# Optimization experiments

Hardware: AMD Instinct MI355X
Metric: run time of the kernel (lower is better)

## Reference

```python
import jax, jax.numpy as jnp
import numpy as np

B, S, IN, E, H, FF, L = 8, 1024, 128, 512, 8, 2048, 4
HD = E // H
EPS = 1e-5


def make_pe(seq_len, d_model):
    position = np.arange(seq_len, dtype=np.float32)[:, None]
    div_term = np.exp(np.arange(0, d_model, 2, dtype=np.float32) * (-np.log(10000.0) / d_model))
    pe = np.zeros((seq_len, d_model), dtype=np.float32)
    pe[:, 0::2] = np.sin(position * div_term)
    pe[:, 1::2] = np.cos(position * div_term)
    return jnp.asarray(pe)


def setup_inputs() -> dict:
    key = jax.random.key(0)
    ks = jax.random.split(key, 16)
    s = 0.02
    return {
        "src": jax.random.normal(ks[0], (B, S, IN), jnp.float32),
        "distances": jax.random.uniform(ks[1], (B, S, S), jnp.float32),
        "proj_w": jax.random.normal(ks[2], (E, IN), jnp.float32) * s,
        "proj_b": jnp.zeros((E,), jnp.float32),
        "bn_g": jnp.ones((E,), jnp.float32),
        "bn_b": jnp.zeros((E,), jnp.float32),
        "in_proj_w": jax.random.normal(ks[3], (3 * E, E), jnp.float32) * s,
        "in_proj_b": jnp.zeros((3 * E,), jnp.float32),
        "dist_scale": jnp.array(1.0, jnp.float32),
        "lin1_w": jax.random.normal(ks[4], (FF, E), jnp.float32) * s,
        "lin1_b": jnp.zeros((FF,), jnp.float32),
        "lin2_w": jax.random.normal(ks[5], (E, FF), jnp.float32) * s,
        "lin2_b": jnp.zeros((E,), jnp.float32),
        "n1_g": jnp.ones((E,), jnp.float32),
        "n1_b": jnp.zeros((E,), jnp.float32),
        "n2_g": jnp.ones((E,), jnp.float32),
        "n2_b": jnp.zeros((E,), jnp.float32),
    }


def layernorm(x, g, b):
    m = jnp.mean(x, axis=-1, keepdims=True)
    v = jnp.var(x, axis=-1, keepdims=True)
    return (x - m) * jax.lax.rsqrt(v + EPS) * g + b


def reference(src, distances, proj_w, proj_b, bn_g, bn_b, in_proj_w, in_proj_b,
              dist_scale, lin1_w, lin1_b, lin2_w, lin2_b, n1_g, n1_b, n2_g, n2_b):
    # input projection
    x = jnp.einsum('bsi,ei->bse', src, proj_w) + proj_b  # [B,S,E]
    # BatchNorm1d over flattened (B*S) dim, training-mode batch stats
    xf = x.reshape(-1, E)
    mu = jnp.mean(xf, axis=0)
    var = jnp.var(xf, axis=0)
    x = ((xf - mu) * jax.lax.rsqrt(var + EPS) * bn_g + bn_b).reshape(B, S, E)
    # positional encoding
    x = x + make_pe(S, E)[None]
    # distance bias (same for every layer)
    dmax = jnp.max(distances, axis=-1, keepdims=True)
    dist_bias = jnp.exp(dist_scale * (1.0 - distances / dmax))  # [B,S,S]
    scale = 1.0 / jnp.sqrt(jnp.float32(HD))
    # num_layers iterations of the SAME (shared-parameter) layer
    for _ in range(L):
        qkv = jnp.einsum('bse,fe->bsf', x, in_proj_w) + in_proj_b  # [B,S,3E]
        q, k, v = jnp.split(qkv, 3, axis=-1)
        q = q.reshape(B, S, H, HD).transpose(0, 2, 1, 3)
        k = k.reshape(B, S, H, HD).transpose(0, 2, 1, 3)
        scores = jnp.einsum('bhqd,bhkd->bhqk', q, k) * scale  # [B,H,S,S]
        attn = jax.nn.softmax(scores, axis=-1)
        avg_w = jnp.mean(attn, axis=1)  # head-averaged weights [B,S,S]
        w = avg_w * dist_bias
        w = w / jnp.sum(w, axis=-1, keepdims=True)
        # NOTE: original bmm uses raw layer input as value (no V/out projection)
        attn_out = jnp.einsum('bqk,bke->bqe', w, x)
        x = layernorm(x + attn_out, n1_g, n1_b)
        ff = jnp.einsum('bsf,ef->bse', jax.nn.relu(jnp.einsum('bse,fe->bsf', x, lin1_w) + lin1_b), lin2_w) + lin2_b
        x = layernorm(x + ff, n2_g, n2_b)
    return x
```

## Files before the change

### kernel.cpp

```cpp
#include <hip/hip_runtime.h>
#include <hip/hip_bf16.h>
#include <math.h>

#define Bz 8
#define Sz 1024
#define INz 128
#define Ez 512
#define Hz 8
#define HDz 64
#define FFz 2048
#define Lz 4
#define Nz (Bz*Sz)
#define EPSf 1e-5f

typedef __attribute__((ext_vector_type(8))) short short8;
typedef __attribute__((ext_vector_type(4))) float floatx4;
#define MFMA16(a,b,c) __builtin_amdgcn_mfma_f32_16x16x32_bf16(a,b,c,0,0,0)

typedef __hip_bfloat16 bf16;

__device__ inline float b2f(bf16 v) { return __bfloat162float(v); }
__device__ inline bf16 f2b(float v) { return __float2bfloat16(v); }
__device__ inline float us2f(unsigned short u) { return __uint_as_float((unsigned)u << 16); }

__device__ inline void gload16(const bf16* g, bf16* lds_base)
{
  __builtin_amdgcn_global_load_lds(
      (const __attribute__((address_space(1))) void*)g,
      (__attribute__((address_space(3))) void*)lds_base,
      16, 0, 0);
}

#define FENCE() asm volatile("" ::: "memory")
#define PB() do { FENCE(); __builtin_amdgcn_s_barrier(); FENCE(); } while (0)
#define VMCNT0() asm volatile("s_waitcnt vmcnt(0)" ::: "memory")
#define VMCNT8() asm volatile("s_waitcnt vmcnt(8)" ::: "memory")

__global__ __launch_bounds__(256) void cast_f2b(const float* __restrict__ in,
    bf16* __restrict__ out, int n)
{
  int i = blockIdx.x * 256 + threadIdx.x;
  if (i < n) out[i] = f2b(in[i]);
}

__global__ __launch_bounds__(512, 1) void gemm256(
    const bf16* __restrict__ A, const bf16* __restrict__ Wm,
    const float* __restrict__ bias, bf16* __restrict__ Cb,
    int N, int K, int relu)
{
  int gx = gridDim.x, nwg = gx * gridDim.y;
  int flat = blockIdx.y * gx + blockIdx.x;
  if (!(nwg & 7)) {
    int cpx = nwg >> 3;
    flat = (flat & 7) * cpx + (flat >> 3);
  }
  int bm = (flat / gx) * 256, bn = (flat % gx) * 256;
  __shared__ __align__(16) bf16 As0[256][64], Bs0[256][64];
  __shared__ __align__(16) bf16 As1[256][64], Bs1[256][64];
  int t = threadIdx.x, wave = t >> 6, lane = t & 63;
  int wm = (wave >> 2) * 128, wn = (wave & 3) * 64;
  int fr = lane & 15, fo = lane >> 4;
  int w8 = wave * 8, lrow = lane >> 3;
  int sc8 = ((lane & 7) ^ (lrow & 7)) * 8;
  floatx4 acc[8][4];
  #pragma unroll
  for (int i = 0; i < 8; ++i)
    #pragma unroll
    for (int j = 0; j < 4; ++j) acc[i][j] = (floatx4){0.f, 0.f, 0.f, 0.f};

  #define STAGE8(DA, DB, kk) do {                                           \
    _Pragma("unroll")                                                        \
    for (int c_ = 0; c_ < 4; ++c_) {                                         \
      int row_ = c_ * 64 + w8 + lrow;                                        \
      gload16(A  + (size_t)(bm + row_) * K + (kk) + sc8, &DA[c_ * 64 + w8][0]);\
      gload16(Wm + (size_t)(bn + row_) * K + (kk) + sc8, &DB[c_ * 64 + w8][0]);\
    } } while (0)

  #define TILE(AA, BB, SA, SB, kk, DOSTAGE) do {                            \
    _Pragma("unroll")                                                        \
    for (int q_ = 0; q_ < 4; ++q_) {                                         \
      short8 a_[4][2], bf_[2][2];                                            \
      _Pragma("unroll")                                                      \
      for (int j_ = 0; j_ < 4; ++j_) {                                       \
        int row_ = wm + ((q_ >> 1) * 4 + j_) * 16 + fr;                      \
        a_[j_][0] = *(const short8*)&AA[row_][((fo) ^ (fr & 7)) * 8];        \
        a_[j_][1] = *(const short8*)&AA[row_][((4 + fo) ^ (fr & 7)) * 8];    \
      }                                                                      \
      _Pragma("unroll")                                                      \
      for (int g_ = 0; g_ < 2; ++g_) {                                       \
        int row_ = wn + ((q_ & 1) * 2 + g_) * 16 + fr;                       \
        bf_[g_][0] = *(const short8*)&BB[row_][((fo) ^ (fr & 7)) * 8];       \
        bf_[g_][1] = *(const short8*)&BB[row_][((4 + fo) ^ (fr & 7)) * 8];   \
      }                                                                      \
      if ((DOSTAGE) && q_ == 0) STAGE8(SA, SB, kk);                          \
      PB();                                                                  \
      __builtin_amdgcn_s_setprio(1);                                         \
      _Pragma("unroll")                                                      \
      for (int j_ = 0; j_ < 4; ++j_)                                         \
        _Pragma("unroll")                                                    \
        for (int g_ = 0; g_ < 2; ++g_) {                                     \
          int fi_ = (q_ >> 1) * 4 + j_, gi_ = (q_ & 1) * 2 + g_;             \
          acc[fi_][gi_] = MFMA16(a_[j_][0], bf_[g_][0], acc[fi_][gi_]);      \
          acc[fi_][gi_] = MFMA16(a_[j_][1], bf_[g_][1], acc[fi_][gi_]);      \
        }                                                                    \
      __builtin_amdgcn_s_setprio(0);                                         \
      if (q_ == 3) VMCNT0();                                                 \
      PB();                                                                  \
    } } while (0)

  int nt = K >> 6;
  STAGE8(As0, Bs0, 0);
  STAGE8(As1, Bs1, 64);
  VMCNT8();
  PB();
  TILE(As0, Bs0, As0, Bs0, 0, 0);
  for (int i = 1; i + 2 < nt; i += 2) {
    TILE(As1, Bs1, As0, Bs0, (i + 1) * 64, 1);
    TILE(As0, Bs0, As1, Bs1, (i + 2) * 64, 1);
  }
  TILE(As1, Bs1, As0, Bs0, 0, 0);
  #undef STAGE8
  #undef TILE

  #pragma unroll
  for (int f = 0; f < 8; ++f) {
    #pragma unroll
    for (int r = 0; r < 4; ++r) {
      int row = bm + wm + f * 16 + (lane >> 4) * 4 + r;
      #pragma unroll
      for (int g = 0; g < 4; ++g) {
        int col = bn + wn + g * 16 + fr;
        float v = acc[f][g][r] + (bias ? bias[col] : 0.f);
        if (relu) v = fmaxf(v, 0.f);
        Cb[(size_t)row * N + col] = f2b(v);
      }
    }
  }
}

__global__ __launch_bounds__(256) void gemm_bt(
    const bf16* __restrict__ A, const bf16* __restrict__ Wm,
    const float* __restrict__ bias, float* __restrict__ Cf,
    bf16* __restrict__ Cb, const float* __restrict__ rowscale,
    int M, int N, int K, int lda, int ldw,
    long sA, long sW, long sC, long sAk, long sWk, int nkc, int relu)
{
  int z = blockIdx.z;
  int bq = z / nkc, kc = z - bq * nkc;
  A  += (size_t)bq * sA + (size_t)kc * sAk;
  Wm += (size_t)bq * sW + (size_t)kc * sWk;
  if (rowscale) rowscale += (size_t)bq * M;
  size_t cbase = (size_t)bq * sC;
  const float* biasp = (kc == 0) ? bias : nullptr;
  int wrCf = (kc == 0), wrCb = (kc == nkc - 1);
  int bm = blockIdx.y * 128, bn = blockIdx.x * 128;
  __shared__ __align__(16) bf16 As0[128][64], Bs0[128][64];
  __shared__ __align__(16) bf16 As1[128][64], Bs1[128][64];
  int t = threadIdx.x, wave = t >> 6, lane = t & 63;
  int wm = (wave >> 1) * 64, wn = (wave & 1) * 64;
  int fr = lane & 15, fo = lane >> 4;
  int srow = lane >> 3;
  int scol = ((lane & 7) ^ srow) * 8;
  floatx4 acc[4][4];
  #pragma unroll
  for (int i = 0; i < 4; ++i)
    #pragma unroll
    for (int j = 0; j < 4; ++j) acc[i][j] = (floatx4){0.f, 0.f, 0.f, 0.f};

  #define STAGE(Ad, Bd, kk) do {                                            \
    _Pragma("unroll")                                                        \
    for (int i_ = 0; i_ < 4; ++i_) {                                         \
      int chunk_ = wave * 4 + i_;                                            \
      int row_ = chunk_ * 8 + srow;                                          \
      gload16(A  + (size_t)(bm + row_) * lda + (kk) + scol, &Ad[chunk_ * 8][0]);\
      gload16(Wm + (size_t)(bn + row_) * ldw + (kk) + scol, &Bd[chunk_ * 8][0]);\
    } } while (0)

  #define COMPUTE(Ad, Bd) do {                                               \
    _Pragma("unroll")                                                        \
    for (int ks_ = 0; ks_ < 2; ++ks_) {                                      \
      int sw_ = ((ks_ * 4 + fo) ^ (fr & 7)) * 8;                             \
      short8 af_[4], bf_[4];                                                 \
      _Pragma("unroll")                                                      \
      for (int rt_ = 0; rt_ < 4; ++rt_)                                      \
        af_[rt_] = *(const short8*)&Ad[wm + rt_ * 16 + fr][sw_];             \
      _Pragma("unroll")                                                      \
      for (int ct_ = 0; ct_ < 4; ++ct_)                                      \
        bf_[ct_] = *(const short8*)&Bd[wn + ct_ * 16 + fr][sw_];             \
      _Pragma("unroll")                                                      \
      for (int rt_ = 0; rt_ < 4; ++rt_)                                      \
        _Pragma("unroll")                                                    \
        for (int ct_ = 0; ct_ < 4; ++ct_)                                    \
          acc[rt_][ct_] = MFMA16(af_[rt_], bf_[ct_], acc[rt_][ct_]);         \
    } } while (0)

  STAGE(As0, Bs0, 0);
  __syncthreads();
  for (int k0 = 0; k0 < K; k0 += 128) {
    if (k0 + 64 < K) STAGE(As1, Bs1, k0 + 64);
    COMPUTE(As0, Bs0);
    __syncthreads();
    if (k0 + 64 < K) {
      if (k0 + 128 < K) STAGE(As0, Bs0, k0 + 128);
      COMPUTE(As1, Bs1);
      __syncthreads();
    }
  }
  #undef STAGE
  #undef COMPUTE

  #pragma unroll
  for (int rt = 0; rt < 4; ++rt) {
    #pragma unroll
    for (int r = 0; r < 4; ++r) {
      int row = bm + wm + rt * 16 + (lane >> 4) * 4 + r;
      float rs = rowscale ? (1.f / rowscale[row]) : 1.f;
      #pragma unroll
      for (int ct = 0; ct < 4; ++ct) {
        int col = bn + wn + ct * 16 + fr;
        float v = acc[rt][ct][r] + (biasp ? biasp[col] : 0.f);
        if (relu) v = fmaxf(v, 0.f);
        v *= rs;
        if (Cf && wrCf) Cf[cbase + (size_t)row * N + col] = v;
        if (Cb && wrCb) Cb[cbase + (size_t)row * N + col] = f2b(v);
      }
    }
  }
}

__global__ __launch_bounds__(256) void bn_stats(const float* __restrict__ x, float* __restrict__ st)
{
  int c = blockIdx.x;
  float s = 0.f, q = 0.f;
  for (int r = threadIdx.x; r < Nz; r += 256) {
    float v = x[(size_t)r * Ez + c];
    s += v; q += v * v;
  }
  for (int o = 32; o; o >>= 1) { s += __shfl_down(s, o); q += __shfl_down(q, o); }
  __shared__ float shs[4], shq[4];
  int w = threadIdx.x >> 6;
  if ((threadIdx.x & 63) == 0) { shs[w] = s; shq[w] = q; }
  __syncthreads();
  if (threadIdx.x == 0) {
    s = shs[0] + shs[1] + shs[2] + shs[3];
    q = shq[0] + shq[1] + shq[2] + shq[3];
    float mu = s / (float)Nz;
    float var = q / (float)Nz - mu * mu;
    st[c] = mu;
    st[Ez + c] = rsqrtf(var + EPSf);
  }
}

__global__ __launch_bounds__(256) void bn_apply_pe(const float* __restrict__ x0,
    const float* __restrict__ st, const float* __restrict__ g,
    const float* __restrict__ b, float* __restrict__ x, bf16* __restrict__ xb)
{
  int idx = blockIdx.x * 256 + threadIdx.x;
  int c = idx & (Ez - 1);
  int r = idx >> 9;
  int s = r & (Sz - 1);
  float dt = expf((float)(c & ~1) * (-9.210340371976184f / (float)Ez));
  float ang = (float)s * dt;
  float pe = (c & 1) ? cosf(ang) : sinf(ang);
  float mu = st[c], rs = st[Ez + c];
  float v = (x0[idx] - mu) * rs * g[c] + b[c] + pe;
  x[idx] = v;
  xb[idx] = f2b(v);
}

__global__ __launch_bounds__(256) void dist_bias_k(const float* __restrict__ dist,
    const float* __restrict__ dsc, bf16* __restrict__ db)
{
  size_t base = (size_t)blockIdx.x * Sz;
  float m = -1e30f;
  for (int j = threadIdx.x; j < Sz; j += 256) m = fmaxf(m, dist[base + j]);
  for (int o = 32; o; o >>= 1) m = fmaxf(m, __shfl_down(m, o));
  __shared__ float sh[4];
  if ((threadIdx.x & 63) == 0) sh[threadIdx.x >> 6] = m;
  __syncthreads();
  m = fmaxf(fmaxf(sh[0], sh[1]), fmaxf(sh[2], sh[3]));
  float sc = dsc[0];
  float inv = 1.f / m;
  for (int j = threadIdx.x; j < Sz; j += 256)
    db[base + j] = f2b(expf(sc * (1.f - dist[base + j] * inv)));
}

__global__ __launch_bounds__(256) void transpose_xb(const bf16* __restrict__ xb,
    bf16* __restrict__ xT)
{
  int b = blockIdx.z, e0 = blockIdx.y * 32, s0 = blockIdx.x * 32;
  __shared__ bf16 T[32][40];
  int t = threadIdx.x, row = t >> 3, c = t & 7;
  *(ushort4*)&T[row][c * 4] = *(const ushort4*)(xb + (size_t)(b * Sz + s0 + row) * Ez + e0 + c * 4);
  __syncthreads();
  ushort4 v;
  unsigned short* vp = (unsigned short*)&v;
  #pragma unroll
  for (int i = 0; i < 4; ++i) vp[i] = *(const unsigned short*)&T[c * 4 + i][row];
  *(ushort4*)(xT + ((size_t)b * Ez + e0 + row) * Sz + s0 + c * 4) = v;
}

__global__ __launch_bounds__(256) void attn_stats2(const bf16* __restrict__ qk,
    float* __restrict__ stats, float* __restrict__ den)
{
  int qt = blockIdx.x, h = blockIdx.y, b = blockIdx.z;
  int q0 = qt * 64;
  int t = threadIdx.x, wave = t >> 6, lane = t & 63;
  if (h == 0 && t < 64) den[(size_t)b * Sz + q0 + t] = 0.f;
  __shared__ bf16 Qs[64][72];
  __shared__ bf16 Ks[128][72];
  int fr = lane & 15, fo = (lane >> 4) * 8;
  #pragma unroll
  for (int i = 0; i < 2; ++i) {
    int idx = i * 256 + t, row = idx >> 3, c4 = idx & 7;
    *(float4*)&Qs[row][c4 * 8] =
      *(const float4*)(qk + (size_t)(b * Sz + q0 + row) * 1024 + h * 64 + c4 * 8);
  }
  __syncthreads();
  short8 aq0 = *(const short8*)&Qs[wave * 16 + fr][fo];
  short8 aq1 = *(const short8*)&Qs[wave * 16 + fr][32 + fo];
  float m_run[4] = {-1e30f, -1e30f, -1e30f, -1e30f};
  float z_run[4] = {0.f, 0.f, 0.f, 0.f};
  for (int k0 = 0; k0 < Sz; k0 += 128) {
    __syncthreads();
    #pragma unroll
    for (int i = 0; i < 4; ++i) {
      int idx = i * 256 + t, row = idx >> 3, c4 = idx & 7;
      *(float4*)&Ks[row][c4 * 8] =
        *(const float4*)(qk + (size_t)(b * Sz + k0 + row) * 1024 + 512 + h * 64 + c4 * 8);
    }
    __syncthreads();
    float sc[8][4];
    #pragma unroll
    for (int j = 0; j < 8; ++j) {
      floatx4 a4 = (floatx4){0.f, 0.f, 0.f, 0.f};
      short8 b0 = *(const short8*)&Ks[j * 16 + fr][fo];
      short8 b1 = *(const short8*)&Ks[j * 16 + fr][32 + fo];
      a4 = MFMA16(aq0, b0, a4);
      a4 = MFMA16(aq1, b1, a4);
      #pragma unroll
      for (int r = 0; r < 4; ++r) sc[j][r] = a4[r] * 0.125f;
    }
    #pragma unroll
    for (int r = 0; r < 4; ++r) {
      float vm = sc[0][r];
      #pragma unroll
      for (int j = 1; j < 8; ++j) vm = fmaxf(vm, sc[j][r]);
      #pragma unroll
      for (int o = 1; o < 16; o <<= 1) vm = fmaxf(vm, __shfl_xor(vm, o, 16));
      float mn = fmaxf(m_run[r], vm);
      float zb = 0.f;
      #pragma unroll
      for (int j = 0; j < 8; ++j) zb += __expf(sc[j][r] - mn);
      #pragma unroll
      for (int o = 1; o < 16; o <<= 1) zb += __shfl_xor(zb, o, 16);
      z_run[r] = z_run[r] * __expf(m_run[r] - mn) + zb;
      m_run[r] = mn;
    }
  }
  if (fr == 0) {
    int qb = q0 + wave * 16 + (lane >> 4) * 4;
    #pragma unroll
    for (int r = 0; r < 4; ++r) {
      size_t o = ((size_t)(b * Hz + h) * Sz + qb + r) * 2;
      stats[o] = m_run[r];
      stats[o + 1] = z_run[r];
    }
  }
}

__global__ __launch_bounds__(256) void scores_bias(const bf16* __restrict__ qk,
    const bf16* __restrict__ db, const float* __restrict__ stats,
    bf16* __restrict__ aw, float* __restrict__ den)
{
  int kt = blockIdx.x, qt = blockIdx.y, b = blockIdx.z;
  int q0 = qt * 128, k0 = kt * 128;
  __shared__ __align__(16) bf16 Qs0[128][64], Ks0[128][64];
  __shared__ __align__(16) bf16 Qs1[128][64], Ks1[128][64];
  __shared__ float mS[128][9];
  __shared__ float ziS[128][9];
  int t = threadIdx.x, wave = t >> 6, lane = t & 63;
  int fr = lane & 15, fo = lane >> 4;
  int wm = (wave >> 1) * 64, wn = (wave & 1) * 64;
  int srow = lane >> 3;
  int scol = ((lane & 7) ^ srow) * 8;
  int sw0 = ((fo) ^ (fr & 7)) * 8, sw1 = ((4 + fo) ^ (fr & 7)) * 8;

  #pragma unroll
  for (int i = 0; i < 4; ++i) {
    int lin = i * 256 + t, h = lin >> 7, q = lin & 127;
    const float* sp = stats + ((size_t)(b * Hz + h) * Sz + q0 + q) * 2;
    mS[q][h] = sp[0];
    ziS[q][h] = 1.f / sp[1];
  }

  floatx4 pac[4][4];
  #pragma unroll
  for (int i = 0; i < 4; ++i)
    #pragma unroll
    for (int j = 0; j < 4; ++j) pac[i][j] = (floatx4){0.f, 0.f, 0.f, 0.f};

  #define STAGEH(Qd, Kd, hh) do {                                            \
    _Pragma("unroll")                                                        \
    for (int i_ = 0; i_ < 4; ++i_) {                                         \
      int chunk_ = wave * 4 + i_, row_ = chunk_ * 8 + srow;                  \
      gload16(qk + (size_t)(b * Sz + q0 + row_) * 1024 + (hh) * 64 + scol,   \
              &Qd[chunk_ * 8][0]);                                           \
      gload16(qk + (size_t)(b * Sz + k0 + row_) * 1024 + 512 + (hh) * 64 + scol,\
              &Kd[chunk_ * 8][0]);                                           \
    } } while (0)

  #define HCOMP(Qd, Kd, hh) do {                                             \
    short8 bfv0[4], bfv1[4];                                                 \
    _Pragma("unroll")                                                        \
    for (int ct = 0; ct < 4; ++ct) {                                         \
      bfv0[ct] = *(const short8*)&Kd[wn + ct * 16 + fr][sw0];                \
      bfv1[ct] = *(const short8*)&Kd[wn + ct * 16 + fr][sw1];                \
    }                                                                        \
    _Pragma("unroll")                                                        \
    for (int rt = 0; rt < 4; ++rt) {                                         \
      short8 af0 = *(const short8*)&Qd[wm + rt * 16 + fr][sw0];              \
      short8 af1 = *(const short8*)&Qd[wm + rt * 16 + fr][sw1];              \
      floatx4 sc[4];                                                         \
      _Pragma("unroll")                                                      \
      for (int ct = 0; ct < 4; ++ct) {                                       \
        floatx4 z4 = (floatx4){0.f, 0.f, 0.f, 0.f};                          \
        z4 = MFMA16(af0, bfv0[ct], z4);                                      \
        sc[ct] = MFMA16(af1, bfv1[ct], z4);                                  \
      }                                                                      \
      _Pragma("unroll")                                                      \
      for (int r = 0; r < 4; ++r) {                                          \
        int qloc = wm + rt * 16 + (lane >> 4) * 4 + r;                       \
        float m = mS[qloc][hh], zi = ziS[qloc][hh];                          \
        _Pragma("unroll")                                                    \
        for (int ct = 0; ct < 4; ++ct)                                       \
          pac[rt][ct][r] += __expf(sc[ct][r] * 0.125f - m) * zi;             \
      }                                                                      \
    } } while (0)

  STAGEH(Qs0, Ks0, 0);
  __syncthreads();
  #pragma unroll 1
  for (int h = 0; h < 8; h += 2) {
    STAGEH(Qs1, Ks1, h + 1);
    HCOMP(Qs0, Ks0, h);
    __syncthreads();
    if (h + 2 < 8) STAGEH(Qs0, Ks0, h + 2);
    HCOMP(Qs1, Ks1, h + 1);
    __syncthreads();
  }
  #undef STAGEH
  #undef HCOMP

  #pragma unroll
  for (int rt = 0; rt < 4; ++rt) {
    #pragma unroll
    for (int r = 0; r < 4; ++r) {
      int qloc = wm + rt * 16 + (lane >> 4) * 4 + r;
      size_t rowoff = (size_t)(b * Sz + q0 + qloc) * Sz + k0;
      float rsum = 0.f;
      #pragma unroll
      for (int ct = 0; ct < 4; ++ct) {
        int kloc = wn + ct * 16 + fr;
        float p = pac[rt][ct][r] * 0.125f * b2f(db[rowoff + kloc]);
        aw[rowoff + kloc] = f2b(p);
        rsum += p;
      }
      #pragma unroll
      for (int o = 1; o < 16; o <<= 1) rsum += __shfl_xor(rsum, o, 16);
      if (fr == 0) atomicAdd(den + (size_t)b * Sz + q0 + qloc, rsum);
    }
  }
}

__global__ __launch_bounds__(256) void add_ln(const float* __restrict__ xin,
    const float* __restrict__ dly, const bf16* __restrict__ dly2,
    const float* __restrict__ g, const float* __restrict__ bb,
    float* __restrict__ xout, bf16* __restrict__ xbout)
{
  size_t base = (size_t)blockIdx.x * Ez;
  int t = threadIdx.x;
  float2 xi = *(const float2*)(xin + base + t * 2);
  float2 dl = *(const float2*)(dly + base + t * 2);
  float a0 = xi.x + dl.x;
  float a1 = xi.y + dl.y;
  if (dly2) {
    ushort2 u = *(const ushort2*)(dly2 + base + t * 2);
    a0 += us2f(u.x);
    a1 += us2f(u.y);
  }
  float s = a0 + a1, q = a0 * a0 + a1 * a1;
  for (int o = 32; o; o >>= 1) { s += __shfl_down(s, o); q += __shfl_down(q, o); }
  __shared__ float shs[4], shq[4];
  if ((t & 63) == 0) { shs[t >> 6] = s; shq[t >> 6] = q; }
  __syncthreads();
  s = shs[0] + shs[1] + shs[2] + shs[3];
  q = shq[0] + shq[1] + shq[2] + shq[3];
  float mu = s * (1.f / Ez);
  float var = q * (1.f / Ez) - mu * mu;
  float rs = rsqrtf(var + EPSf);
  float v0 = (a0 - mu) * rs * g[t * 2] + bb[t * 2];
  float v1 = (a1 - mu) * rs * g[t * 2 + 1] + bb[t * 2 + 1];
  float2 vo; vo.x = v0; vo.y = v1;
  *(float2*)(xout + base + t * 2) = vo;
  bf16 b0 = f2b(v0), b1 = f2b(v1);
  ushort2 pk;
  pk.x = *(unsigned short*)&b0;
  pk.y = *(unsigned short*)&b1;
  *(ushort2*)(xbout + base + t * 2) = pk;
}

extern "C" void kernel_launch(void* const* d_in, const int* in_sizes, int n_in,
                              void* d_out, int out_size, void* d_ws, size_t ws_size,
                              hipStream_t stream)
{
  const float* src        = (const float*)d_in[0];
  const float* distances  = (const float*)d_in[1];
  const float* proj_w     = (const float*)d_in[2];
  const float* proj_b     = (const float*)d_in[3];
  const float* bn_g       = (const float*)d_in[4];
  const float* bn_b       = (const float*)d_in[5];
  const float* in_proj_w  = (const float*)d_in[6];
  const float* in_proj_b  = (const float*)d_in[7];
  const float* dist_scale = (const float*)d_in[8];
  const float* lin1_w     = (const float*)d_in[9];
  const float* lin1_b     = (const float*)d_in[10];
  const float* lin2_w     = (const float*)d_in[11];
  const float* lin2_b     = (const float*)d_in[12];
  const float* n1_g       = (const float*)d_in[13];
  const float* n1_b       = (const float*)d_in[14];
  const float* n2_g       = (const float*)d_in[15];
  const float* n2_b       = (const float*)d_in[16];

  float* x = (float*)d_out;

  float* stats = (float*)d_ws;
  float* den   = stats + 131072;
  float* bnst  = den + 8192;
  float* aout  = bnst + 1024;
  float* x0    = aout;
  bf16* db_b = (bf16*)(aout + (size_t)Nz * Ez);
  bf16* Rqk  = db_b + (size_t)Bz * Sz * Sz;
  bf16* qk   = Rqk;
  bf16* aw   = Rqk + (size_t)Nz * 1024;
  bf16* ff1  = Rqk;
  bf16* xb   = Rqk + (size_t)Nz * FFz;
  bf16* xT   = xb + (size_t)Nz * Ez;
  bf16* srcb = xT + (size_t)Bz * Ez * Sz;
  bf16* wpr  = srcb + (size_t)Nz * INz;
  bf16* wqk  = wpr + Ez * INz;
  bf16* wl1  = wqk + 1024 * Ez;
  bf16* wl2  = wl1 + FFz * Ez;
  bf16* pvs2 = qk;
  bf16* ffs2 = xT;

  cast_f2b<<<(Nz * INz) / 256, 256, 0, stream>>>(src, srcb, Nz * INz);
  cast_f2b<<<(Ez * INz + 255) / 256, 256, 0, stream>>>(proj_w, wpr, Ez * INz);
  cast_f2b<<<(1024 * Ez) / 256, 256, 0, stream>>>(in_proj_w, wqk, 1024 * Ez);
  cast_f2b<<<(FFz * Ez) / 256, 256, 0, stream>>>(lin1_w, wl1, FFz * Ez);
  cast_f2b<<<(Ez * FFz) / 256, 256, 0, stream>>>(lin2_w, wl2, Ez * FFz);

  gemm_bt<<<dim3(Ez / 128, Nz / 128, 1), 256, 0, stream>>>(
      srcb, wpr, proj_b, x0, nullptr, nullptr,
      Nz, Ez, INz, INz, INz, 0, 0, 0, 0, 0, 1, 0);
  bn_stats<<<Ez, 256, 0, stream>>>(x0, bnst);
  bn_apply_pe<<<(Nz * Ez) / 256, 256, 0, stream>>>(x0, bnst, bn_g, bn_b, x, xb);
  dist_bias_k<<<Bz * Sz, 256, 0, stream>>>(distances, dist_scale, db_b);

  for (int l = 0; l < Lz; ++l) {
    transpose_xb<<<dim3(Sz / 32, Ez / 32, Bz), 256, 0, stream>>>(xb, xT);
    gemm_bt<<<dim3(1024 / 128, Nz / 128, 1), 256, 0, stream>>>(
        xb, wqk, in_proj_b, nullptr, qk, nullptr,
        Nz, 1024, Ez, Ez, Ez, 0, 0, 0, 0, 0, 1, 0);
    attn_stats2<<<dim3(Sz / 64, Hz, Bz), 256, 0, stream>>>(qk, stats, den);
    scores_bias<<<dim3(Sz / 128, Sz / 128, Bz), 256, 0, stream>>>(qk, db_b, stats, aw, den);
    gemm_bt<<<dim3(Ez / 128, Sz / 128, Bz * 2), 256, 0, stream>>>(
        aw, xT, nullptr, aout, pvs2, den,
        Sz, Ez, 512, Sz, Sz,
        (long)Sz * Sz, (long)Ez * Sz, (long)Sz * Ez, 512, 512, 2, 0);
    add_ln<<<Nz, 256, 0, stream>>>(x, aout, pvs2, n1_g, n1_b, x, xb);
    gemm256<<<dim3(FFz / 256, Nz / 256), 512, 0, stream>>>(
        xb, wl1, lin1_b, ff1, FFz, Ez, 1);
    gemm_bt<<<dim3(Ez / 128, Nz / 128, 2), 256, 0, stream>>>(
        ff1, wl2, lin2_b, aout, ffs2, nullptr,
        Nz, Ez, 1024, FFz, FFz, 0, 0, 0, 1024, 1024, 2, 0);
    add_ln<<<Nz, 256, 0, stream>>>(x, aout, ffs2, n2_g, n2_b, x, xb);
  }
}
```

Measured before the change: 1.147 ms.

## Double query rows per attn_stats block and drop split-K in PV and FF2 GEMMs

attn_stats2 now gives each wave two 16-row query groups, so one block covers 128 queries and each K tile loaded into shared memory is reused twice. This halves the grid and the K-tile global traffic. The PV and FF2 GEMMs no longer use a 2-way split-K with a bf16 partial buffer summed in add_ln; each now runs a single full-K pass. This removes the partial-sum writes and reads but halves the number of blocks for those GEMMs and lengthens the per-block K loop.

Result: slower. 1.189 ms (+3.7%).

```diff
diff --git a/kernel.cpp b/kernel.cpp
--- a/kernel.cpp
+++ b/kernel.cpp
@@ -304,23 +304,32 @@
     float* __restrict__ stats, float* __restrict__ den)
 {
   int qt = blockIdx.x, h = blockIdx.y, b = blockIdx.z;
-  int q0 = qt * 64;
+  int q0 = qt * 128;
   int t = threadIdx.x, wave = t >> 6, lane = t & 63;
-  if (h == 0 && t < 64) den[(size_t)b * Sz + q0 + t] = 0.f;
-  __shared__ bf16 Qs[64][72];
+  if (h == 0 && t < 128) den[(size_t)b * Sz + q0 + t] = 0.f;
+  __shared__ bf16 Qs[128][72];
   __shared__ bf16 Ks[128][72];
   int fr = lane & 15, fo = (lane >> 4) * 8;
   #pragma unroll
-  for (int i = 0; i < 2; ++i) {
+  for (int i = 0; i < 4; ++i) {
     int idx = i * 256 + t, row = idx >> 3, c4 = idx & 7;
     *(float4*)&Qs[row][c4 * 8] =
       *(const float4*)(qk + (size_t)(b * Sz + q0 + row) * 1024 + h * 64 + c4 * 8);
   }
   __syncthreads();
-  short8 aq0 = *(const short8*)&Qs[wave * 16 + fr][fo];
-  short8 aq1 = *(const short8*)&Qs[wave * 16 + fr][32 + fo];
-  float m_run[4] = {-1e30f, -1e30f, -1e30f, -1e30f};
-  float z_run[4] = {0.f, 0.f, 0.f, 0.f};
+  short8 aq0[2], aq1[2];
+  #pragma unroll
+  for (int g = 0; g < 2; ++g) {
+    int row = wave * 32 + g * 16 + fr;
+    aq0[g] = *(const short8*)&Qs[row][fo];
+    aq1[g] = *(const short8*)&Qs[row][32 + fo];
+  }
+  float m_run[2][4], z_run[2][4];
+  #pragma unroll
+  for (int g = 0; g < 2; ++g)
+    #pragma unroll
+    for (int r = 0; r < 4; ++r) { m_run[g][r] = -1e30f; z_run[g][r] = 0.f; }
+
   for (int k0 = 0; k0 < Sz; k0 += 128) {
     __syncthreads();
     #pragma unroll
@@ -330,41 +339,47 @@
         *(const float4*)(qk + (size_t)(b * Sz + k0 + row) * 1024 + 512 + h * 64 + c4 * 8);
     }
     __syncthreads();
-    float sc[8][4];
-    #pragma unroll
-    for (int j = 0; j < 8; ++j) {
-      floatx4 a4 = (floatx4){0.f, 0.f, 0.f, 0.f};
-      short8 b0 = *(const short8*)&Ks[j * 16 + fr][fo];
-      short8 b1 = *(const short8*)&Ks[j * 16 + fr][32 + fo];
-      a4 = MFMA16(aq0, b0, a4);
-      a4 = MFMA16(aq1, b1, a4);
+    #pragma unroll
+    for (int g = 0; g < 2; ++g) {
+      float sc[8][4];
       #pragma unroll
-      for (int r = 0; r < 4; ++r) sc[j][r] = a4[r] * 0.125f;
+      for (int j = 0; j < 8; ++j) {
+        floatx4 a4 = (floatx4){0.f, 0.f, 0.f, 0.f};
+        short8 b0 = *(const short8*)&Ks[j * 16 + fr][fo];
+        short8 b1 = *(const short8*)&Ks[j * 16 + fr][32 + fo];
+        a4 = MFMA16(aq0[g], b0, a4);
+        a4 = MFMA16(aq1[g], b1, a4);
+        #pragma unroll
+        for (int r = 0; r < 4; ++r) sc[j][r] = a4[r] * 0.125f;
+      }
+      #pragma unroll
+      for (int r = 0; r < 4; ++r) {
+        float vm = sc[0][r];
+        #pragma unroll
+        for (int j = 1; j < 8; ++j) vm = fmaxf(vm, sc[j][r]);
+        #pragma unroll
+        for (int o = 1; o < 16; o <<= 1) vm = fmaxf(vm, __shfl_xor(vm, o, 16));
+        float mn = fmaxf(m_run[g][r], vm);
+        float zb = 0.f;
+        #pragma unroll
+        for (int j = 0; j < 8; ++j) zb += __expf(sc[j][r] - mn);
+        #pragma unroll
+        for (int o = 1; o < 16; o <<= 1) zb += __shfl_xor(zb, o, 16);
+        z_run[g][r] = z_run[g][r] * __expf(m_run[g][r] - mn) + zb;
+        m_run[g][r] = mn;
+      }
     }
-    #pragma unroll
-    for (int r = 0; r < 4; ++r) {
-      float vm = sc[0][r];
+  }
+  if (fr == 0) {
+    #pragma unroll
+    for (int g = 0; g < 2; ++g) {
+      int qb = q0 + wave * 32 + g * 16 + (lane >> 4) * 4;
       #pragma unroll
-      for (int j = 1; j < 8; ++j) vm = fmaxf(vm, sc[j][r]);
-      #pragma unroll
-      for (int o = 1; o < 16; o <<= 1) vm = fmaxf(vm, __shfl_xor(vm, o, 16));
-      float mn = fmaxf(m_run[r], vm);
-      float zb = 0.f;
-      #pragma unroll
-      for (int j = 0; j < 8; ++j) zb += __expf(sc[j][r] - mn);
-      #pragma unroll
-      for (int o = 1; o < 16; o <<= 1) zb += __shfl_xor(zb, o, 16);
-      z_run[r] = z_run[r] * __expf(m_run[r] - mn) + zb;
-      m_run[r] = mn;
-    }
-  }
-  if (fr == 0) {
-    int qb = q0 + wave * 16 + (lane >> 4) * 4;
-    #pragma unroll
-    for (int r = 0; r < 4; ++r) {
-      size_t o = ((size_t)(b * Hz + h) * Sz + qb + r) * 2;
-      stats[o] = m_run[r];
-      stats[o + 1] = z_run[r];
+      for (int r = 0; r < 4; ++r) {
+        size_t o = ((size_t)(b * Hz + h) * Sz + qb + r) * 2;
+        stats[o] = m_run[g][r];
+        stats[o + 1] = z_run[g][r];
+      }
     }
   }
 }
@@ -551,8 +566,6 @@
   bf16* wqk  = wpr + Ez * INz;
   bf16* wl1  = wqk + 1024 * Ez;
   bf16* wl2  = wl1 + FFz * Ez;
-  bf16* pvs2 = qk;
-  bf16* ffs2 = xT;
 
   cast_f2b<<<(Nz * INz) / 256, 256, 0, stream>>>(src, srcb, Nz * INz);
   cast_f2b<<<(Ez * INz + 255) / 256, 256, 0, stream>>>(proj_w, wpr, Ez * INz);
@@ -572,18 +585,18 @@
     gemm_bt<<<dim3(1024 / 128, Nz / 128, 1), 256, 0, stream>>>(
         xb, wqk, in_proj_b, nullptr, qk, nullptr,
         Nz, 1024, Ez, Ez, Ez, 0, 0, 0, 0, 0, 1, 0);
-    attn_stats2<<<dim3(Sz / 64, Hz, Bz), 256, 0, stream>>>(qk, stats, den);
+    attn_stats2<<<dim3(Sz / 128, Hz, Bz), 256, 0, stream>>>(qk, stats, den);
     scores_bias<<<dim3(Sz / 128, Sz / 128, Bz), 256, 0, stream>>>(qk, db_b, stats, aw, den);
-    gemm_bt<<<dim3(Ez / 128, Sz / 128, Bz * 2), 256, 0, stream>>>(
-        aw, xT, nullptr, aout, pvs2, den,
-        Sz, Ez, 512, Sz, Sz,
-        (long)Sz * Sz, (long)Ez * Sz, (long)Sz * Ez, 512, 512, 2, 0);
-    add_ln<<<Nz, 256, 0, stream>>>(x, aout, pvs2, n1_g, n1_b, x, xb);
+    gemm_bt<<<dim3(Ez / 128, Sz / 128, Bz), 256, 0, stream>>>(
+        aw, xT, nullptr, aout, nullptr, den,
+        Sz, Ez, Sz, Sz, Sz,
+        (long)Sz * Sz, (long)Ez * Sz, (long)Sz * Ez, 0, 0, 1, 0);
+    add_ln<<<Nz, 256, 0, stream>>>(x, aout, nullptr, n1_g, n1_b, x, xb);
     gemm256<<<dim3(FFz / 256, Nz / 256), 512, 0, stream>>>(
         xb, wl1, lin1_b, ff1, FFz, Ez, 1);
-    gemm_bt<<<dim3(Ez / 128, Nz / 128, 2), 256, 0, stream>>>(
-        ff1, wl2, lin2_b, aout, ffs2, nullptr,
-        Nz, Ez, 1024, FFz, FFz, 0, 0, 0, 1024, 1024, 2, 0);
-    add_ln<<<Nz, 256, 0, stream>>>(x, aout, ffs2, n2_g, n2_b, x, xb);
-  }
-}
+    gemm_bt<<<dim3(Ez / 128, Nz / 128, 1), 256, 0, stream>>>(
+        ff1, wl2, lin2_b, aout, nullptr, nullptr,
+        Nz, Ez, FFz, FFz, FFz, 0, 0, 0, 0, 0, 1, 0);
+    add_ln<<<Nz, 256, 0, stream>>>(x, aout, nullptr, n2_g, n2_b, x, xb);
+  }
+}
```
